# Kernel tuning notes

Measured on AMD Instinct MI355X. Metric: run time of the kernel, lower is better.

The kernel has to match this reference:

```python
import jax, jax.numpy as jnp
import numpy as np

BIG = 1e8  # > max possible squared distance in a 64^3 volume (3*63^2 ~ 1.2e4)


def _edt(mask):
    """Exact Euclidean distance transform (scipy.ndimage.distance_transform_edt).

    mask: [B, X, Y, Z] float; distance at nonzero voxels to nearest zero voxel.
    Uses the exact separable squared-EDT: along each axis,
      g[i] = min_j f[j] + (i - j)^2  (lower envelope of parabolas, brute-forced).
    """
    f = jnp.where(mask > 0, BIG, 0.0).astype(jnp.float32)
    for ax in (1, 2, 3):
        f = jnp.moveaxis(f, ax, -1)            # [..., n]
        n = f.shape[-1]
        i = jnp.arange(n)
        d2 = ((i[:, None] - i[None, :]) ** 2).astype(jnp.float32)  # [n, n]
        f = jnp.min(f[..., None, :] + d2, axis=-1)                 # [..., n]
        f = jnp.moveaxis(f, -1, ax)
    return jnp.sqrt(f)


def _get_dist_map(mmap, label_inner, label_outer):
    lz = jnp.isin(mmap, jnp.asarray(label_outer)).astype(jnp.float32)
    lz = jnp.where(jnp.isin(mmap, jnp.asarray(label_inner)), 0.0, lz)
    tdm_outer = _edt(lz)                       # distance inside outer region to its zero set
    b = _edt(1.0 - lz)
    boundary = jnp.where(b == 1.0, 1.0, 0.0)   # boundary[boundary != 1] = 0
    outer = tdm_outer + boundary
    level_zero_inner = (outer == 0.0).astype(jnp.float32)
    tsd = -_edt(level_zero_inner) + tdm_outer  # signed distance
    return boundary, tsd


def setup_inputs() -> dict:
    key = jax.random.key(0)
    mmap = jax.random.randint(key, (2, 64, 64, 64), 0, 10, dtype=jnp.int32)
    return {"mmap": mmap}


def reference(mmap):
    d_mean = 2.0
    inner_boundary, phi_inner = _get_dist_map(mmap, [3, 5, 6, 7, 8, 9], [2, 1, 4, 0])
    outer_boundary, phi_outer = _get_dist_map(mmap, [3, 5, 6, 7, 8, 9, 2], [1, 4, 0])
    hausdorff_inner = jnp.abs(inner_boundary * phi_outer)
    hausdorff_outer = jnp.abs(outer_boundary * phi_inner)
    h_in_mean = hausdorff_inner.sum() / inner_boundary.sum()
    h_out_mean = hausdorff_outer.sum() / outer_boundary.sum()
    loss = (h_in_mean - d_mean) ** 2 + (h_out_mean - d_mean) ** 2
    return (h_in_mean, hausdorff_inner.max(), h_out_mean, hausdorff_outer.max(), loss)
```

## Files before the change

kernel.cpp:

```cpp
#include <hip/hip_runtime.h>
#include <math.h>

#define N 64
#define PLANE 4096
#define MASK1 0x17u
#define MASK2 0x13u
#define SENT 16000
typedef unsigned long long ull;

#define CX_OFF ((size_t)0)
#define ML_OFF ((size_t)131072)
#define BD_OFF ((size_t)262144)
#define PART_OFF ((size_t)393216)
#define CTR_OFF (PART_OFF + (size_t)256 * 8 * 4)

__global__ __launch_bounds__(512) void build_bits(const int* __restrict__ mmap,
                                                  void* __restrict__ wsv) {
  __shared__ unsigned char colb[2][8][64];
  const int bid = blockIdx.x;
  const int b = bid >> 6, x = bid & 63;
  const int t = threadIdx.x;
  const int z = t & 63, c = t >> 6;
  if (bid == 0 && t < 2) ((int*)((char*)wsv + CTR_OFF))[t] = 0;
  const size_t pb = (size_t)(b * N + x) * PLANE;
  unsigned b1 = 0, b2 = 0;
  #pragma unroll
  for (int k = 0; k < 8; ++k) {
    const int v = mmap[pb + (8 * c + k) * N + z];
    b1 |= ((MASK1 >> v) & 1u) << k;
    b2 |= ((MASK2 >> v) & 1u) << k;
  }
  colb[0][c][z] = (unsigned char)b1;
  colb[1][c][z] = (unsigned char)b2;
  __syncthreads();
  if (t < 128) {
    const int mm = t >> 6, zz = t & 63;
    ull v = 0;
    #pragma unroll
    for (int cc = 0; cc < 8; ++cc)
      v |= (ull)colb[mm][cc][zz] << (8 * cc);
    ((ull*)((char*)wsv + CX_OFF))[(size_t)(mm * 2 + b) * 4096 + x * 64 + zz] = v;
  }
}

__global__ __launch_bounds__(512) void stencil_k(void* __restrict__ wsv) {
  const int idx = blockIdx.x * 512 + threadIdx.x;
  const int mi = idx >> 12, ci = idx & 4095;
  const int x = ci >> 6, z = ci & 63;
  const ull* cx = (const ull*)((char*)wsv + CX_OFF) + (size_t)mi * 4096;
  const ull c0 = cx[ci];
  const ull xm = (x > 0) ? cx[ci - 64] : 0ull;
  const ull xp = (x < 63) ? cx[ci + 64] : 0ull;
  const ull zm = (z > 0) ? cx[ci - 1] : 0ull;
  const ull zp = (z < 63) ? cx[ci + 1] : 0ull;
  const ull nb = xm | xp | zm | zp | (c0 << 1) | (c0 >> 1);
  ((ull*)((char*)wsv + ML_OFF))[(size_t)mi * 4096 + ci] = c0 | nb;
  ((ull*)((char*)wsv + BD_OFF))[(size_t)mi * 4096 + ci] = nb & ~c0;
}

__global__ __launch_bounds__(512) void edt_all(void* __restrict__ wsv,
                                               float* __restrict__ out) {
  __shared__ unsigned int g1p[64][65];
  __shared__ unsigned int g2p[64][67];
  __shared__ float redS[8], redB[8], redM[8];
  __shared__ int lastFlag;
  const int bid = blockIdx.x;
  const int m = bid >> 7;
  const int mi = bid >> 6;
  const int y0 = bid & 63;
  const int t = threadIdx.x;

  const ull* cxO = (const ull*)((char*)wsv + CX_OFF) + (size_t)mi * 4096;
  const ull* mLO = (const ull*)((char*)wsv + ML_OFF) + (size_t)mi * 4096;
  const ull* bndP = (const ull*)((char*)wsv + BD_OFF) +
                    (size_t)((1 - m) * 2 + (mi & 1)) * 4096;

  #pragma unroll
  for (int k = 0; k < 8; ++k) {
    const int ci = t + 512 * k;
    const int z = ci & 63;
    const ull mT = ~cxO[ci];
    const ull mLw = mLO[ci];
    const int zs = z * z;
    unsigned vT, vL;
    {
      const ull hi = mT >> y0;
      const int du = hi ? (__ffsll((long long)hi) - 1) : 99;
      const int dd = (int)__clzll((long long)(mT << (63 - y0)));
      const int d = min(du, dd);
      vT = (d > 63) ? (unsigned)SENT : (unsigned)(d * d + zs);
    }
    {
      const ull hi = mLw >> y0;
      const int du = hi ? (__ffsll((long long)hi) - 1) : 99;
      const int dd = (int)__clzll((long long)(mLw << (63 - y0)));
      const int d = min(du, dd);
      vL = (d > 63) ? (unsigned)SENT : (unsigned)(d * d + zs);
    }
    g1p[ci >> 6][z] = vT | (vL << 16);
  }
  __syncthreads();

  {
    const int x = t >> 3, g = t & 7;
    unsigned acc[8], n2i[8];
    #pragma unroll
    for (int q = 0; q < 8; ++q) {
      acc[q] = 0x7FFF7FFFu;
      n2i[q] = (unsigned)(unsigned short)(-2 * (g + 8 * q)) * 0x10001u;
    }
    unsigned jp = 0;
    const unsigned* row = &g1p[x][0];
    #pragma unroll 4
    for (int j = 0; j < 64; ++j) {
      const unsigned fj = row[j];
      #pragma unroll
      for (int q = 0; q < 8; ++q) {
        unsigned d;
        asm("v_pk_mad_i16 %0, %1, %2, %3"
            : "=v"(d) : "v"(n2i[q]), "v"(jp), "v"(fj));
        asm("v_pk_min_i16 %0, %1, %2"
            : "=v"(acc[q]) : "v"(acc[q]), "v"(d));
      }
      jp += 0x10001u;
    }
    const int xs = x * x;
    #pragma unroll
    for (int q = 0; q < 8; ++q) {
      const int zp = g + 8 * q;
      const unsigned spk = (unsigned)(zp * zp + xs) * 0x10001u;
      unsigned gv;
      asm("v_pk_add_i16 %0, %1, %2" : "=v"(gv) : "v"(acc[q]), "v"(spk));
      g2p[zp][x] = gv;
    }
  }
  __syncthreads();

  {
    const int z = t >> 3, g = t & 7;
    unsigned acc[8], n2i[8];
    #pragma unroll
    for (int q = 0; q < 8; ++q) {
      acc[q] = 0x7FFF7FFFu;
      n2i[q] = (unsigned)(unsigned short)(-2 * (g + 8 * q)) * 0x10001u;
    }
    unsigned jp = 0;
    const unsigned* row = &g2p[z][0];
    #pragma unroll 4
    for (int j = 0; j < 64; ++j) {
      const unsigned fj = row[j];
      #pragma unroll
      for (int q = 0; q < 8; ++q) {
        unsigned d;
        asm("v_pk_mad_i16 %0, %1, %2, %3"
            : "=v"(d) : "v"(n2i[q]), "v"(jp), "v"(fj));
        asm("v_pk_min_i16 %0, %1, %2"
            : "=v"(acc[q]) : "v"(acc[q]), "v"(d));
      }
      jp += 0x10001u;
    }
    float hsum = 0.f, bsum = 0.f, hmax = 0.f;
    #pragma unroll
    for (int q = 0; q < 8; ++q) {
      const int xp = g + 8 * q;
      const int xs2 = xp * xp;
      const int eT = (int)(short)(acc[q] & 0xFFFFu) + xs2;
      const int eL = (int)(short)(acc[q] >> 16) + xs2;
      const float tsd = sqrtf((float)eT) - sqrtf((float)eL);
      const float bnd = (float)((bndP[xp * 64 + z] >> y0) & 1ull);
      const float h = bnd * fabsf(tsd);
      hsum += h; bsum += bnd; hmax = fmaxf(hmax, h);
    }
    #pragma unroll
    for (int o = 32; o > 0; o >>= 1) {
      hsum += __shfl_down(hsum, o);
      bsum += __shfl_down(bsum, o);
      hmax = fmaxf(hmax, __shfl_down(hmax, o));
    }
    const int w = t >> 6;
    if ((t & 63) == 0) { redS[w] = hsum; redB[w] = bsum; redM[w] = hmax; }
  }
  __syncthreads();

  float* part = (float*)((char*)wsv + PART_OFF);
  int* ctr = (int*)((char*)wsv + CTR_OFF);
  if (t == 0) {
    float s = 0.f, bs = 0.f, mx = 0.f;
    #pragma unroll
    for (int i = 0; i < 8; ++i) {
      s += redS[i]; bs += redB[i]; mx = fmaxf(mx, redM[i]);
    }
    float* p = part + (size_t)bid * 8;
    p[0] = s; p[1] = bs; p[2] = mx;
    __threadfence();
    const int old = atomicAdd(ctr, 1);
    lastFlag = (old == 255) ? 1 : 0;
  }
  __syncthreads();
  if (lastFlag) {
    __threadfence();
    float s = 0.f, bs = 0.f, mx = 0.f;
    if (t < 256) {
      const float* p = part + (size_t)t * 8;
      s = p[0]; bs = p[1]; mx = p[2];
    }
    #pragma unroll
    for (int o = 32; o > 0; o >>= 1) {
      s += __shfl_down(s, o);
      bs += __shfl_down(bs, o);
      mx = fmaxf(mx, __shfl_down(mx, o));
    }
    __syncthreads();
    if ((t & 63) == 0 && t < 256) {
      redS[t >> 6] = s; redB[t >> 6] = bs; redM[t >> 6] = mx;
    }
    __syncthreads();
    if (t == 0) {
      const float s_ho = redS[0] + redS[1], b2 = redB[0] + redB[1];
      const float mho = fmaxf(redM[0], redM[1]);
      const float s_hi = redS[2] + redS[3], b1 = redB[2] + redB[3];
      const float mhi = fmaxf(redM[2], redM[3]);
      const float him = s_hi / b1;
      const float hom = s_ho / b2;
      out[0] = him;
      out[1] = mhi;
      out[2] = hom;
      out[3] = mho;
      out[4] = (him - 2.f) * (him - 2.f) + (hom - 2.f) * (hom - 2.f);
    }
  }
}

extern "C" void kernel_launch(void* const* d_in, const int* in_sizes, int n_in,
                              void* d_out, int out_size, void* d_ws,
                              size_t ws_size, hipStream_t stream) {
  (void)in_sizes; (void)n_in; (void)out_size; (void)ws_size;
  const int* mmap = (const int*)d_in[0];
  float* out = (float*)d_out;

  build_bits<<<128, 512, 0, stream>>>(mmap, d_ws);
  stencil_k<<<32, 512, 0, stream>>>(d_ws);
  edt_all<<<256, 512, 0, stream>>>(d_ws, out);
}
```

Before: 34.03 us.

## Fuse bit-building, stencil and EDT into one kernel with grid barrier

Merges the three kernels into a single 256-block kernel. Each block first builds half a plane of bitmasks, then waits on a global atomic-counter grid barrier before loading two full bit volumes into shared memory. The stencil dilation and boundary masks are recomputed per block from LDS, and the boundary column is gathered via ballot instead of being read from global memory. This removes two launches and the global ML/BD buffers, but adds a spin barrier that depends on all 256 blocks being co-resident, a memset launch, and redundant per-block stencil work.

```diff
diff --git a/kernel.cpp b/kernel.cpp
--- a/kernel.cpp
+++ b/kernel.cpp
@@ -9,78 +9,89 @@
 typedef unsigned long long ull;
 
 #define CX_OFF ((size_t)0)
-#define ML_OFF ((size_t)131072)
-#define BD_OFF ((size_t)262144)
-#define PART_OFF ((size_t)393216)
+#define PART_OFF ((size_t)131072)
 #define CTR_OFF (PART_OFF + (size_t)256 * 8 * 4)
 
-__global__ __launch_bounds__(512) void build_bits(const int* __restrict__ mmap,
-                                                  void* __restrict__ wsv) {
+__global__ __launch_bounds__(512) void hausdorff_one(
+    const int* __restrict__ mmap, void* __restrict__ wsv,
+    float* __restrict__ out) {
+  __shared__ ull cxO[4096];
+  __shared__ ull cxP[4096];
+  __shared__ unsigned g1p[64][65];
   __shared__ unsigned char colb[2][8][64];
-  const int bid = blockIdx.x;
-  const int b = bid >> 6, x = bid & 63;
-  const int t = threadIdx.x;
-  const int z = t & 63, c = t >> 6;
-  if (bid == 0 && t < 2) ((int*)((char*)wsv + CTR_OFF))[t] = 0;
-  const size_t pb = (size_t)(b * N + x) * PLANE;
-  unsigned b1 = 0, b2 = 0;
-  #pragma unroll
-  for (int k = 0; k < 8; ++k) {
-    const int v = mmap[pb + (8 * c + k) * N + z];
-    b1 |= ((MASK1 >> v) & 1u) << k;
-    b2 |= ((MASK2 >> v) & 1u) << k;
-  }
-  colb[0][c][z] = (unsigned char)b1;
-  colb[1][c][z] = (unsigned char)b2;
-  __syncthreads();
-  if (t < 128) {
-    const int mm = t >> 6, zz = t & 63;
-    ull v = 0;
-    #pragma unroll
-    for (int cc = 0; cc < 8; ++cc)
-      v |= (ull)colb[mm][cc][zz] << (8 * cc);
-    ((ull*)((char*)wsv + CX_OFF))[(size_t)(mm * 2 + b) * 4096 + x * 64 + zz] = v;
-  }
-}
-
-__global__ __launch_bounds__(512) void stencil_k(void* __restrict__ wsv) {
-  const int idx = blockIdx.x * 512 + threadIdx.x;
-  const int mi = idx >> 12, ci = idx & 4095;
-  const int x = ci >> 6, z = ci & 63;
-  const ull* cx = (const ull*)((char*)wsv + CX_OFF) + (size_t)mi * 4096;
-  const ull c0 = cx[ci];
-  const ull xm = (x > 0) ? cx[ci - 64] : 0ull;
-  const ull xp = (x < 63) ? cx[ci + 64] : 0ull;
-  const ull zm = (z > 0) ? cx[ci - 1] : 0ull;
-  const ull zp = (z < 63) ? cx[ci + 1] : 0ull;
-  const ull nb = xm | xp | zm | zp | (c0 << 1) | (c0 >> 1);
-  ((ull*)((char*)wsv + ML_OFF))[(size_t)mi * 4096 + ci] = c0 | nb;
-  ((ull*)((char*)wsv + BD_OFF))[(size_t)mi * 4096 + ci] = nb & ~c0;
-}
-
-__global__ __launch_bounds__(512) void edt_all(void* __restrict__ wsv,
-                                               float* __restrict__ out) {
-  __shared__ unsigned int g1p[64][65];
-  __shared__ unsigned int g2p[64][67];
+  __shared__ ull bndCol[64];
   __shared__ float redS[8], redB[8], redM[8];
   __shared__ int lastFlag;
+
   const int bid = blockIdx.x;
+  const int t = threadIdx.x;
+  const int z = t & 63;
+  ull* cxg = (ull*)((char*)wsv + CX_OFF);
+  int* ctr = (int*)((char*)wsv + CTR_OFF);
+
+  {
+    const int p = bid >> 1, h = bid & 1;
+    const int c = t >> 6;
+    const size_t pb = (size_t)p * PLANE;
+    unsigned n1 = 0, n2 = 0;
+    #pragma unroll
+    for (int k = 0; k < 4; ++k) {
+      const int v = mmap[pb + (32 * h + 4 * c + k) * N + z];
+      n1 |= ((MASK1 >> v) & 1u) << k;
+      n2 |= ((MASK2 >> v) & 1u) << k;
+    }
+    colb[0][c][z] = (unsigned char)n1;
+    colb[1][c][z] = (unsigned char)n2;
+    __syncthreads();
+    if (t < 128) {
+      const int mm = t >> 6, zz = t & 63;
+      unsigned half = 0;
+      #pragma unroll
+      for (int cc = 0; cc < 8; ++cc)
+        half |= (unsigned)colb[mm][cc][zz] << (4 * cc);
+      const int b = p >> 6, x = p & 63;
+      ((unsigned*)cxg)[((size_t)(mm * 2 + b) * 4096 + x * 64 + zz) * 2 + h] =
+          half;
+    }
+  }
+
+  __syncthreads();
+  if (t == 0) {
+    __threadfence();
+    atomicAdd(&ctr[0], 1);
+    while (__hip_atomic_load(&ctr[0], __ATOMIC_ACQUIRE,
+                             __HIP_MEMORY_SCOPE_AGENT) < 256) {
+      __builtin_amdgcn_s_sleep(2);
+    }
+    __threadfence();
+  }
+  __syncthreads();
+
   const int m = bid >> 7;
   const int mi = bid >> 6;
   const int y0 = bid & 63;
-  const int t = threadIdx.x;
-
-  const ull* cxO = (const ull*)((char*)wsv + CX_OFF) + (size_t)mi * 4096;
-  const ull* mLO = (const ull*)((char*)wsv + ML_OFF) + (size_t)mi * 4096;
-  const ull* bndP = (const ull*)((char*)wsv + BD_OFF) +
-                    (size_t)((1 - m) * 2 + (mi & 1)) * 4096;
+  const int miP = ((1 - m) << 1) | (mi & 1);
 
   #pragma unroll
   for (int k = 0; k < 8; ++k) {
     const int ci = t + 512 * k;
-    const int z = ci & 63;
-    const ull mT = ~cxO[ci];
-    const ull mLw = mLO[ci];
+    cxO[ci] = cxg[(size_t)mi * 4096 + ci];
+    cxP[ci] = cxg[(size_t)miP * 4096 + ci];
+  }
+  __syncthreads();
+
+  #pragma unroll
+  for (int k = 0; k < 8; ++k) {
+    const int ci = t + 512 * k;
+    const int x = ci >> 6;
+    const ull c0 = cxO[ci];
+    const ull xm = (x > 0) ? cxO[ci - 64] : 0ull;
+    const ull xp = (x < 63) ? cxO[ci + 64] : 0ull;
+    const ull zm = (z > 0) ? cxO[ci - 1] : 0ull;
+    const ull zp = (z < 63) ? cxO[ci + 1] : 0ull;
+    const ull nb = xm | xp | zm | zp | (c0 << 1) | (c0 >> 1);
+    const ull mT = ~c0;
+    const ull mLw = c0 | nb;
     const int zs = z * z;
     unsigned vT, vL;
     {
@@ -97,9 +108,20 @@
       const int d = min(du, dd);
       vL = (d > 63) ? (unsigned)SENT : (unsigned)(d * d + zs);
     }
-    g1p[ci >> 6][z] = vT | (vL << 16);
-  }
-  __syncthreads();
+    g1p[x][z] = vT | (vL << 16);
+    const ull p0 = cxP[ci];
+    const ull pxm = (x > 0) ? cxP[ci - 64] : 0ull;
+    const ull pxp = (x < 63) ? cxP[ci + 64] : 0ull;
+    const ull pzm = (z > 0) ? cxP[ci - 1] : 0ull;
+    const ull pzp = (z < 63) ? cxP[ci + 1] : 0ull;
+    const ull pnb = pxm | pxp | pzm | pzp | (p0 << 1) | (p0 >> 1);
+    const int bit = (int)(((pnb & ~p0) >> y0) & 1ull);
+    const ull bal = __ballot(bit);
+    if (z == 0) bndCol[x] = bal;
+  }
+  __syncthreads();
+
+  unsigned* g2p = (unsigned*)cxP;
 
   {
     const int x = t >> 3, g = t & 7;
@@ -119,25 +141,24 @@
         unsigned d;
         asm("v_pk_mad_i16 %0, %1, %2, %3"
             : "=v"(d) : "v"(n2i[q]), "v"(jp), "v"(fj));
-        asm("v_pk_min_i16 %0, %1, %2"
-            : "=v"(acc[q]) : "v"(acc[q]), "v"(d));
+        asm("v_pk_min_i16 %0, %1, %2" : "=v"(acc[q]) : "v"(acc[q]), "v"(d));
       }
       jp += 0x10001u;
     }
     const int xs = x * x;
     #pragma unroll
     for (int q = 0; q < 8; ++q) {
-      const int zp = g + 8 * q;
-      const unsigned spk = (unsigned)(zp * zp + xs) * 0x10001u;
+      const int zpr = g + 8 * q;
+      const unsigned spk = (unsigned)(zpr * zpr + xs) * 0x10001u;
       unsigned gv;
       asm("v_pk_add_i16 %0, %1, %2" : "=v"(gv) : "v"(acc[q]), "v"(spk));
-      g2p[zp][x] = gv;
+      g2p[zpr * 67 + x] = gv;
     }
   }
   __syncthreads();
 
   {
-    const int z = t >> 3, g = t & 7;
+    const int zc = t >> 3, g = t & 7;
     unsigned acc[8], n2i[8];
     #pragma unroll
     for (int q = 0; q < 8; ++q) {
@@ -145,7 +166,7 @@
       n2i[q] = (unsigned)(unsigned short)(-2 * (g + 8 * q)) * 0x10001u;
     }
     unsigned jp = 0;
-    const unsigned* row = &g2p[z][0];
+    const unsigned* row = &g2p[zc * 67];
     #pragma unroll 4
     for (int j = 0; j < 64; ++j) {
       const unsigned fj = row[j];
@@ -154,20 +175,19 @@
         unsigned d;
         asm("v_pk_mad_i16 %0, %1, %2, %3"
             : "=v"(d) : "v"(n2i[q]), "v"(jp), "v"(fj));
-        asm("v_pk_min_i16 %0, %1, %2"
-            : "=v"(acc[q]) : "v"(acc[q]), "v"(d));
+        asm("v_pk_min_i16 %0, %1, %2" : "=v"(acc[q]) : "v"(acc[q]), "v"(d));
       }
       jp += 0x10001u;
     }
     float hsum = 0.f, bsum = 0.f, hmax = 0.f;
     #pragma unroll
     for (int q = 0; q < 8; ++q) {
-      const int xp = g + 8 * q;
-      const int xs2 = xp * xp;
+      const int xpr = g + 8 * q;
+      const int xs2 = xpr * xpr;
       const int eT = (int)(short)(acc[q] & 0xFFFFu) + xs2;
       const int eL = (int)(short)(acc[q] >> 16) + xs2;
       const float tsd = sqrtf((float)eT) - sqrtf((float)eL);
-      const float bnd = (float)((bndP[xp * 64 + z] >> y0) & 1ull);
+      const float bnd = (float)((bndCol[xpr] >> zc) & 1ull);
       const float h = bnd * fabsf(tsd);
       hsum += h; bsum += bnd; hmax = fmaxf(hmax, h);
     }
@@ -183,17 +203,16 @@
   __syncthreads();
 
   float* part = (float*)((char*)wsv + PART_OFF);
-  int* ctr = (int*)((char*)wsv + CTR_OFF);
   if (t == 0) {
     float s = 0.f, bs = 0.f, mx = 0.f;
     #pragma unroll
     for (int i = 0; i < 8; ++i) {
       s += redS[i]; bs += redB[i]; mx = fmaxf(mx, redM[i]);
     }
-    float* p = part + (size_t)bid * 8;
-    p[0] = s; p[1] = bs; p[2] = mx;
-    __threadfence();
-    const int old = atomicAdd(ctr, 1);
+    float* pp = part + (size_t)bid * 8;
+    pp[0] = s; pp[1] = bs; pp[2] = mx;
+    __threadfence();
+    const int old = atomicAdd(&ctr[1], 1);
     lastFlag = (old == 255) ? 1 : 0;
   }
   __syncthreads();
@@ -201,8 +220,8 @@
     __threadfence();
     float s = 0.f, bs = 0.f, mx = 0.f;
     if (t < 256) {
-      const float* p = part + (size_t)t * 8;
-      s = p[0]; bs = p[1]; mx = p[2];
+      const float* pp = part + (size_t)t * 8;
+      s = pp[0]; bs = pp[1]; mx = pp[2];
     }
     #pragma unroll
     for (int o = 32; o > 0; o >>= 1) {
@@ -238,7 +257,6 @@
   const int* mmap = (const int*)d_in[0];
   float* out = (float*)d_out;
 
-  build_bits<<<128, 512, 0, stream>>>(mmap, d_ws);
-  stencil_k<<<32, 512, 0, stream>>>(d_ws);
-  edt_all<<<256, 512, 0, stream>>>(d_ws, out);
+  hipMemsetAsync((char*)d_ws + CTR_OFF, 0, 8, stream);
+  hausdorff_one<<<256, 512, 0, stream>>>(mmap, d_ws, out);
 }
```

Measured after the change: 53.71 us. 1.58x slower.
